# Performance work log

Measured on AMD Instinct MI355X. Metric: run time of the kernel, lower is better.

## Reference

```python
import jax, jax.numpy as jnp
import numpy as np

B, S, V, E, H = 64, 512, 32000, 512, 1024


def setup_inputs() -> dict:
    key = jax.random.key(0)
    ks = jax.random.split(key, 8)
    s = 1.0 / np.sqrt(H).astype(np.float32)
    x = jax.random.randint(ks[0], (B, S), 0, V)  # token ids
    h0 = jnp.zeros((B, H), jnp.float32)
    c0 = jnp.zeros((B, H), jnp.float32)
    emb = jax.random.normal(ks[1], (V, E), jnp.float32) * 0.02
    W_ih = jax.random.uniform(ks[2], (4 * H, E), jnp.float32, -s, s)
    W_hh = jax.random.uniform(ks[3], (4 * H, H), jnp.float32, -s, s)
    b_ih = jax.random.uniform(ks[4], (4 * H,), jnp.float32, -s, s)
    b_hh = jax.random.uniform(ks[5], (4 * H,), jnp.float32, -s, s)
    fc_w = jax.random.uniform(ks[6], (1, H), jnp.float32, -s, s)
    fc_b = jax.random.uniform(ks[7], (1,), jnp.float32, -s, s)
    return {"x": x, "h0": h0, "c0": c0, "emb": emb, "W_ih": W_ih,
            "W_hh": W_hh, "b_ih": b_ih, "b_hh": b_hh, "fc_w": fc_w, "fc_b": fc_b}


def reference(x, h0, c0, emb, W_ih, W_hh, b_ih, b_hh, fc_w, fc_b):
    embeds = emb[x]                      # [B, S, E]
    xs = jnp.swapaxes(embeds, 0, 1)      # [S, B, E] for scan over time
    # precompute input projections for all timesteps in one big GEMM
    xproj = jnp.einsum('sbe,ge->sbg', xs, W_ih) + b_ih  # [S, B, 4H]

    def step(carry, xg):
        h, c = carry
        gates = xg + h @ W_hh.T + b_hh   # [B, 4H], torch LSTMCell gate order i,f,g,o
        i, f, g, o = jnp.split(gates, 4, axis=-1)
        c2 = jax.nn.sigmoid(f) * c + jax.nn.sigmoid(i) * jnp.tanh(g)
        h2 = jax.nn.sigmoid(o) * jnp.tanh(c2)
        return (h2, c2), None

    (h, c), _ = jax.lax.scan(step, (h0, c0), xproj)
    # dropout is identity in eval mode
    out = h @ fc_w.T + fc_b              # [B, 1]
    sig = jax.nn.sigmoid(out)
    sig_out = sig.reshape(x.shape[0], -1)[:, -1]  # [B]
    return (sig_out, h, c)
```

## Files before the change

### kernel.cpp

```cpp
#include <hip/hip_runtime.h>

typedef unsigned short u16;
typedef unsigned int   u32;

typedef __bf16 bf16x8 __attribute__((ext_vector_type(8)));
typedef float  f32x4  __attribute__((ext_vector_type(4)));

#define NB   64
#define NS   512
#define NE   512
#define NH   1024
#define NK   1536
#define NV   32000

#define WPKF_BYTES  12582912u
#define HFRAG_BYTES 262144u
#define AEMBF_BYTES 33554432u
#define BSUM_BYTES  16384u
#define BAR_BYTES   32768u

__device__ __forceinline__ u16 f2bf(float f) {
    u32 u = __builtin_bit_cast(u32, f);
    u += 0x7fffu + ((u >> 16) & 1u);
    return (u16)(u >> 16);
}
__device__ __forceinline__ bf16x8 pack8(float4 a, float4 b) {
    union { u16 u[8]; bf16x8 v; } o;
    o.u[0]=f2bf(a.x); o.u[1]=f2bf(a.y); o.u[2]=f2bf(a.z); o.u[3]=f2bf(a.w);
    o.u[4]=f2bf(b.x); o.u[5]=f2bf(b.y); o.u[6]=f2bf(b.z); o.u[7]=f2bf(b.w);
    return o.v;
}
__device__ __forceinline__ float sigf(float x) {
    return __frcp_rn(1.0f + __expf(-x));
}
__device__ __forceinline__ float tanhf_fast(float x) {
    return 1.0f - 2.0f * __frcp_rn(__expf(2.0f * x) + 1.0f);
}
__device__ __forceinline__ int clamptok(int t) {
    return t < 0 ? 0 : (t >= NV ? NV - 1 : t);
}

__global__ void __launch_bounds__(256)
prep_fused(const int* __restrict__ x, const float* __restrict__ emb,
           const float* __restrict__ Wih, const float* __restrict__ Whh,
           const float* __restrict__ bih, const float* __restrict__ bhh,
           const float* __restrict__ h0,
           u16* __restrict__ wpkf, u16* __restrict__ aembf,
           u16* __restrict__ hfrag0, float* __restrict__ bsum,
           unsigned* __restrict__ bar, int tierA)
{
    const int b = blockIdx.x, t = threadIdx.x;
    if (b < 3072) {
        int oblk = b * 2 + (t >> 7);
        int ot   = t & 127;
        int cg = oblk / 48, kt = oblk % 48;
        int f = ot >> 6, lane = ot & 63;
        int n16 = lane & 15, quad = lane >> 4;
        int nl = f * 16 + n16;
        int j = (nl >> 3) * NH + cg * 8 + (nl & 7);
        int k = kt * 32 + quad * 8;
        const float* src = (k < NH) ? (Whh + (size_t)j * NH + k)
                                    : (Wih + (size_t)j * NE + (k - NH));
        union { bf16x8 v; uint4 q; } o;
        o.v = pack8(*(const float4*)src, *(const float4*)(src + 4));
        *(uint4*)(wpkf + (((size_t)oblk * 2 + f) * 64 + lane) * 8) = o.q;
    } else if (b < 5120) {
        if (!tierA) return;
        int oblk = b - 3072;
        int s = oblk >> 2, bg = oblk & 3;
#pragma unroll
        for (int i = 0; i < 4; ++i) {
            int u = t + i * 256;
            int kt16 = u >> 6, lane = u & 63;
            int n16 = lane & 15, quad = lane >> 4;
            int bb = bg * 16 + n16;
            int tok = clamptok(x[bb * NS + s]);
            const float* ep = emb + (size_t)tok * NE + kt16 * 32 + quad * 8;
            union { bf16x8 v; uint4 q; } o;
            o.v = pack8(*(const float4*)ep, *(const float4*)(ep + 4));
            *(uint4*)(aembf + (((size_t)oblk * 16 + kt16) * 64 + lane) * 8) = o.q;
        }
    } else if (b < 5152) {
        int oblk = (b - 5120) * 4 + (t >> 6);
        int lane = t & 63;
        int bg = oblk >> 5, kt = oblk & 31;
        int n16 = lane & 15, quad = lane >> 4;
        int bb = bg * 16 + n16;
        int k = kt * 32 + quad * 8;
        const float* src = h0 + (size_t)bb * NH + k;
        union { bf16x8 v; uint4 q; } o;
        o.v = pack8(*(const float4*)src, *(const float4*)(src + 4));
        *(uint4*)(hfrag0 + ((size_t)oblk * 64 + lane) * 8) = o.q;
    } else {
        int i = (b - 5152) * 256 + t;
        bsum[i] = bih[i] + bhh[i];
        bar[i] = 0u;
        bar[i + 4096] = 0u;
    }
}

__global__ void init_state(const float* __restrict__ h0,
                           const float* __restrict__ c0,
                           float* __restrict__ out) {
    int i = blockIdx.x * 256 + threadIdx.x;
    float* out_h = out + 64;
    float* out_c = out + 64 + NB * NH;
    ((float4*)out_h)[i] = ((const float4*)h0)[i];
    ((float4*)out_c)[i] = ((const float4*)c0)[i];
}

template<bool EMBF>
__device__ __forceinline__ void persist_body(
    const int* __restrict__ x, const float* __restrict__ emb,
    const u16* __restrict__ wpkf, const u16* __restrict__ aembf,
    u16* __restrict__ hf0, u16* __restrict__ hf1,
    const float* __restrict__ bsum, const float* __restrict__ c0,
    float* __restrict__ cstate, float* __restrict__ out_h,
    unsigned* __restrict__ bar)
{
    const int tid  = threadIdx.x;
    const int lane = tid & 63;
    const int w    = tid >> 6;
    const int blk  = blockIdx.x;
    const int cg   = blk & 127;
    const int bgp  = blk >> 7;
    const int quad = lane >> 4;
    const int n16  = lane & 15;

    __shared__ u16   lw[48 * 2 * 64 * 8];
    __shared__ float part[4][32][36];

    {
        const uint4* src = (const uint4*)(wpkf + (size_t)cg * (48 * 2 * 64 * 8));
        uint4* dst = (uint4*)lw;
#pragma unroll
        for (int i = 0; i < 24; ++i)
            dst[i * 256 + tid] = src[i * 256 + tid];
    }

    const int mloc = tid >> 3;
    const int uu   = tid & 7;
    const int be   = bgp * 32 + mloc;
    const int je   = cg * 8 + uu;
    const float bp0 = bsum[0 * NH + je];
    const float bp1 = bsum[1 * NH + je];
    const float bp2 = bsum[2 * NH + je];
    const float bp3 = bsum[3 * NH + je];
    float c_reg = c0[(size_t)be * NH + je];

    const int kth   = cg >> 2;
    const int lane2 = (cg & 3) * 16 + (mloc & 15);
    const int bgW   = bgp * 2 + (mloc >> 4);
    const size_t hwo_base = ((size_t)(bgW * 32 + kth) * 64 + lane2) * 8;

    const int bg0 = bgp * 2, bg1 = bg0 + 1;

    unsigned* my_flag = bar + ((size_t)(bgp * 128 + cg) * 32);
    const unsigned* pw_flag =
        bar + ((size_t)(bgp * 128 + w * 32 + (lane & 31)) * 32);

    bf16x8 ea0[4], ea1[4];
    auto loadE = [&](int s) {
        if (EMBF) {
            const u16* e0 = aembf + ((size_t)(s * 4 + bg0) * 16) * (64 * 8);
            const u16* e1 = aembf + ((size_t)(s * 4 + bg1) * 16) * (64 * 8);
#pragma unroll
            for (int i = 0; i < 4; ++i) {
                int ke = w * 4 + i;
                ea0[i] = *(const bf16x8*)(e0 + ((size_t)ke * 64 + lane) * 8);
                ea1[i] = *(const bf16x8*)(e1 + ((size_t)ke * 64 + lane) * 8);
            }
        } else {
            int t0 = clamptok(x[(bg0 * 16 + n16) * NS + s]);
            int t1 = clamptok(x[(bg1 * 16 + n16) * NS + s]);
            const float* p0 = emb + (size_t)t0 * NE + quad * 8;
            const float* p1 = emb + (size_t)t1 * NE + quad * 8;
#pragma unroll
            for (int i = 0; i < 4; ++i) {
                int ko = (w * 4 + i) * 32;
                ea0[i] = pack8(*(const float4*)(p0 + ko), *(const float4*)(p0 + ko + 4));
                ea1[i] = pack8(*(const float4*)(p1 + ko), *(const float4*)(p1 + ko + 4));
            }
        }
    };
    loadE(0);
    __syncthreads();

#pragma unroll 1
    for (int s = 0; s < NS; ++s) {
        const u16* hb = (s & 1) ? hf1 : hf0;
        u16*       ho = (s & 1) ? hf0 : hf1;
        const u16* hb0 = hb + (size_t)(bg0 * 32) * (64 * 8);
        const u16* hb1 = hb + (size_t)(bg1 * 32) * (64 * 8);

        f32x4 acc00 = {0.f,0.f,0.f,0.f}, acc01 = {0.f,0.f,0.f,0.f};
        f32x4 acc10 = {0.f,0.f,0.f,0.f}, acc11 = {0.f,0.f,0.f,0.f};

        uint4 hv0[8], hv1[8];
#pragma unroll
        for (int i = 0; i < 8; ++i) {
            const u16* a0p = hb0 + ((size_t)((w * 8 + i) * 64 + lane)) * 8;
            const u16* a1p = hb1 + ((size_t)((w * 8 + i) * 64 + lane)) * 8;
            asm volatile("global_load_dwordx4 %0, %1, off sc0 sc1"
                         : "=v"(hv0[i]) : "v"(a0p) : "memory");
            asm volatile("global_load_dwordx4 %0, %1, off sc0 sc1"
                         : "=v"(hv1[i]) : "v"(a1p) : "memory");
        }

#pragma unroll
        for (int i = 0; i < 4; ++i) {
            int kt = 32 + w * 4 + i;
            bf16x8 w0 = *(const bf16x8*)(lw + ((size_t)(kt * 2 + 0) * 64 + lane) * 8);
            bf16x8 w1 = *(const bf16x8*)(lw + ((size_t)(kt * 2 + 1) * 64 + lane) * 8);
            acc00 = __builtin_amdgcn_mfma_f32_16x16x32_bf16(ea0[i], w0, acc00, 0, 0, 0);
            acc01 = __builtin_amdgcn_mfma_f32_16x16x32_bf16(ea0[i], w1, acc01, 0, 0, 0);
            acc10 = __builtin_amdgcn_mfma_f32_16x16x32_bf16(ea1[i], w0, acc10, 0, 0, 0);
            acc11 = __builtin_amdgcn_mfma_f32_16x16x32_bf16(ea1[i], w1, acc11, 0, 0, 0);
        }

        asm volatile("s_waitcnt vmcnt(0)" ::: "memory");
        __builtin_amdgcn_sched_barrier(0);

#pragma unroll
        for (int i = 0; i < 8; ++i) {
            int kt = w * 8 + i;
            bf16x8 a0 = __builtin_bit_cast(bf16x8, hv0[i]);
            bf16x8 a1 = __builtin_bit_cast(bf16x8, hv1[i]);
            bf16x8 w0 = *(const bf16x8*)(lw + ((size_t)(kt * 2 + 0) * 64 + lane) * 8);
            bf16x8 w1 = *(const bf16x8*)(lw + ((size_t)(kt * 2 + 1) * 64 + lane) * 8);
            acc00 = __builtin_amdgcn_mfma_f32_16x16x32_bf16(a0, w0, acc00, 0, 0, 0);
            acc01 = __builtin_amdgcn_mfma_f32_16x16x32_bf16(a0, w1, acc01, 0, 0, 0);
            acc10 = __builtin_amdgcn_mfma_f32_16x16x32_bf16(a1, w0, acc10, 0, 0, 0);
            acc11 = __builtin_amdgcn_mfma_f32_16x16x32_bf16(a1, w1, acc11, 0, 0, 0);
        }

        {
            int mrow = quad * 4;
#pragma unroll
            for (int r = 0; r < 4; ++r) {
                part[w][mrow + r][n16]           = acc00[r];
                part[w][mrow + r][16 + n16]      = acc01[r];
                part[w][16 + mrow + r][n16]      = acc10[r];
                part[w][16 + mrow + r][16 + n16] = acc11[r];
            }
        }
        __syncthreads();

        float hN;
        {
            float gv0 = bp0, gv1 = bp1, gv2 = bp2, gv3 = bp3;
#pragma unroll
            for (int ww = 0; ww < 4; ++ww) {
                gv0 += part[ww][mloc][ 0 + uu];
                gv1 += part[ww][mloc][ 8 + uu];
                gv2 += part[ww][mloc][16 + uu];
                gv3 += part[ww][mloc][24 + uu];
            }
            float iS = sigf(gv0);
            float fS = sigf(gv1);
            float gT = tanhf_fast(gv2);
            float oS = sigf(gv3);
            float c_new = fS * c_reg + iS * gT;
            c_new = fminf(20.0f, fmaxf(-20.0f, c_new));
            c_reg = c_new;
            hN = oS * tanhf_fast(c_new);
        }

        if (s == NS - 1) {
            out_h[(size_t)be * NH + je]  = hN;
            cstate[(size_t)be * NH + je] = c_reg;
        } else {
            const unsigned need = (unsigned)(s + 1);
            u32 hbf = f2bf(hN);
            u32 hup = (u32)__shfl_down((int)hbf, 1);
            if ((uu & 1) == 0) {
                u32 val = hbf | (hup << 16);
                u32* dst = (u32*)(ho + hwo_base + uu);
                __hip_atomic_store(dst, val, __ATOMIC_RELAXED,
                                   __HIP_MEMORY_SCOPE_AGENT);
            }
            asm volatile("s_waitcnt vmcnt(0)" ::: "memory");
            __syncthreads();
            if (tid == 0)
                __hip_atomic_store(my_flag, need, __ATOMIC_RELAXED,
                                   __HIP_MEMORY_SCOPE_AGENT);
            {
                unsigned v;
                while (true) {
                    asm volatile("global_load_dword %0, %1, off sc0 sc1\n\t"
                                 "s_waitcnt vmcnt(0)"
                                 : "=v"(v) : "v"(pw_flag) : "memory");
                    if (__all(v >= need)) break;
                    __builtin_amdgcn_s_sleep(1);
                }
            }
            loadE(s + 1);
        }
    }
}

__global__ void __launch_bounds__(256, 1)
lstm_persist_a(const int* __restrict__ x, const float* __restrict__ emb,
               const u16* __restrict__ wpkf, const u16* __restrict__ aembf,
               u16* __restrict__ hf0, u16* __restrict__ hf1,
               const float* __restrict__ bsum, const float* __restrict__ c0,
               float* __restrict__ cstate, float* __restrict__ out_h,
               unsigned* __restrict__ bar) {
    persist_body<true>(x, emb, wpkf, aembf, hf0, hf1, bsum, c0, cstate, out_h, bar);
}

__global__ void __launch_bounds__(256, 1)
lstm_persist_b(const int* __restrict__ x, const float* __restrict__ emb,
               const u16* __restrict__ wpkf, const u16* __restrict__ aembf,
               u16* __restrict__ hf0, u16* __restrict__ hf1,
               const float* __restrict__ bsum, const float* __restrict__ c0,
               float* __restrict__ cstate, float* __restrict__ out_h,
               unsigned* __restrict__ bar) {
    persist_body<false>(x, emb, wpkf, aembf, hf0, hf1, bsum, c0, cstate, out_h, bar);
}

__global__ void __launch_bounds__(256)
lstm_step_raw(const int* __restrict__ x, const float* __restrict__ emb,
              const float* __restrict__ Wih, const float* __restrict__ Whh,
              const float* __restrict__ bih, const float* __restrict__ bhh,
              const float* __restrict__ hA, float* __restrict__ hB,
              float* __restrict__ cbuf, int s) {
    const int tid  = threadIdx.x;
    const int lane = tid & 63;
    const int w    = tid >> 6;
    const int blk  = blockIdx.x;
    const int cg   = blk & 127;
    const int bg   = blk >> 7;
    const int u0   = cg * 8;
    const int b0   = bg * 16;

    __shared__ float part[4][16][36];
    const int n16 = lane & 15;
    const int kq  = (lane >> 4) * 8;
    const int tok = clamptok(x[(b0 + n16) * NS + s]);

    const int nl0 = n16, nl1 = 16 + n16;
    const int r0 = (nl0 >> 3) * NH + u0 + (nl0 & 7);
    const int r1 = (nl1 >> 3) * NH + u0 + (nl1 & 7);

    f32x4 acc0 = {0.f,0.f,0.f,0.f};
    f32x4 acc1 = {0.f,0.f,0.f,0.f};

#pragma unroll
    for (int tkt = 0; tkt < 12; ++tkt) {
        int kt = w * 12 + tkt;
        int ko = kt * 32 + kq;
        const float *s0, *s1;
        if (kt < 32) { s0 = Whh + (size_t)r0 * NH + ko; s1 = Whh + (size_t)r1 * NH + ko; }
        else         { s0 = Wih + (size_t)r0 * NE + (ko - NH); s1 = Wih + (size_t)r1 * NE + (ko - NH); }
        bf16x8 wf0 = pack8(*(const float4*)s0, *(const float4*)(s0 + 4));
        bf16x8 wf1 = pack8(*(const float4*)s1, *(const float4*)(s1 + 4));
        bf16x8 a0;
        if (kt < 32) {
            const float* hp = hA + (size_t)(b0 + n16) * NH + ko;
            a0 = pack8(*(const float4*)hp, *(const float4*)(hp + 4));
        } else {
            const float* ep = emb + (size_t)tok * NE + (ko - NH);
            a0 = pack8(*(const float4*)ep, *(const float4*)(ep + 4));
        }
        acc0 = __builtin_amdgcn_mfma_f32_16x16x32_bf16(a0, wf0, acc0, 0, 0, 0);
        acc1 = __builtin_amdgcn_mfma_f32_16x16x32_bf16(a0, wf1, acc1, 0, 0, 0);
    }

    {
        int mrow = (lane >> 4) * 4;
#pragma unroll
        for (int r = 0; r < 4; ++r) {
            part[w][mrow + r][n16]      = acc0[r];
            part[w][mrow + r][16 + n16] = acc1[r];
        }
    }
    __syncthreads();

    if (tid < 128) {
        const int mloc = tid >> 3, uu = tid & 7;
        const int be = b0 + mloc, je = u0 + uu;
        float gv[4];
#pragma unroll
        for (int g = 0; g < 4; ++g) {
            int n = g * 8 + uu;
            gv[g] = part[0][mloc][n] + part[1][mloc][n]
                  + part[2][mloc][n] + part[3][mloc][n]
                  + bih[g * NH + je] + bhh[g * NH + je];
        }
        float iS = sigf(gv[0]);
        float fS = sigf(gv[1]);
        float gT = tanhf_fast(gv[2]);
        float oS = sigf(gv[3]);
        float c_new = fS * cbuf[be * NH + je] + iS * gT;
        c_new = fminf(20.0f, fmaxf(-20.0f, c_new));
        float hN = oS * tanhf_fast(c_new);
        cbuf[be * NH + je] = c_new;
        hB[be * NH + je]   = hN;
    }
}

__global__ void final_fc_simple(const float* __restrict__ fc_w,
                                const float* __restrict__ fc_b,
                                float* __restrict__ out) {
    __shared__ float red[64][5];
    const float* out_h = out + 64;
    int t = threadIdx.x;
    int b = t >> 2, q = t & 3;
    const float* hp = out_h + b * NH + q * 256;
    const float* wp = fc_w + q * 256;
    float sacc = 0.f;
#pragma unroll 4
    for (int i = 0; i < 64; ++i) {
        float4 hv = ((const float4*)hp)[i];
        float4 wv = ((const float4*)wp)[i];
        sacc += hv.x * wv.x + hv.y * wv.y + hv.z * wv.z + hv.w * wv.w;
    }
    red[b][q] = sacc;
    __syncthreads();
    if (q == 0) {
        float tot = red[b][0] + red[b][1] + red[b][2] + red[b][3] + fc_b[0];
        out[b] = 1.0f / (1.0f + expf(-tot));
    }
}

extern "C" void kernel_launch(void* const* d_in, const int* in_sizes, int n_in,
                              void* d_out, int out_size, void* d_ws, size_t ws_size,
                              hipStream_t stream) {
    const int*   x   = (const int*)d_in[0];
    const float* h0  = (const float*)d_in[1];
    const float* c0  = (const float*)d_in[2];
    const float* emb = (const float*)d_in[3];
    const float* Wih = (const float*)d_in[4];
    const float* Whh = (const float*)d_in[5];
    const float* bih = (const float*)d_in[6];
    const float* bhh = (const float*)d_in[7];
    const float* fcw = (const float*)d_in[8];
    const float* fcb = (const float*)d_in[9];

    float* out   = (float*)d_out;
    float* out_h = out + 64;
    float* out_c = out + 64 + NB * NH;

    const size_t needA = (size_t)WPKF_BYTES + HFRAG_BYTES + AEMBF_BYTES + BSUM_BYTES + BAR_BYTES;
    const size_t needB = (size_t)WPKF_BYTES + HFRAG_BYTES + BSUM_BYTES + BAR_BYTES;
    const bool tierA = ws_size >= needA;
    const bool tierB = !tierA && ws_size >= needB;

    if (tierA || tierB) {
        u16* wpkf  = (u16*)d_ws;
        u16* hfrag = (u16*)((char*)d_ws + WPKF_BYTES);
        u16* hf0 = hfrag;
        u16* hf1 = hfrag + HFRAG_BYTES / 4;
        char* after = (char*)d_ws + WPKF_BYTES + HFRAG_BYTES;
        u16*   aembf = tierA ? (u16*)after : nullptr;
        float* bsum  = (float*)(after + (tierA ? AEMBF_BYTES : 0));
        unsigned* bar = (unsigned*)((char*)bsum + BSUM_BYTES);

        hipLaunchKernelGGL(prep_fused, dim3(5168), dim3(256), 0, stream,
                           x, emb, Wih, Whh, bih, bhh, h0,
                           wpkf, aembf, hf0, bsum, bar, (int)tierA);

        void* kargs[11] = { &x, &emb, &wpkf, &aembf, &hf0, &hf1,
                            &bsum, &c0, &out_c, &out_h, &bar };
        (void)hipLaunchCooperativeKernel(
            tierA ? reinterpret_cast<const void*>(&lstm_persist_a)
                  : reinterpret_cast<const void*>(&lstm_persist_b),
            dim3(256), dim3(256), kargs, 0u, stream);
    } else {
        hipLaunchKernelGGL(init_state, dim3(64), dim3(256), 0, stream, h0, c0, out);
        float* wsH = (float*)d_ws;
        for (int s = 0; s < NS; ++s) {
            const float* hA = (s & 1) ? wsH : out_h;
            float*       hB = (s & 1) ? out_h : wsH;
            hipLaunchKernelGGL(lstm_step_raw, dim3(512), dim3(256), 0, stream,
                               x, emb, Wih, Whh, bih, bhh, hA, hB, out_c, s);
        }
    }

    hipLaunchKernelGGL(final_fc_simple, dim3(1), dim3(256), 0, stream,
                       fcw, fcb, out);
}
```

Before: 2.046 ms.

## Replace block barrier before flag publish with per-wave flags and double-buffered partials

Each wave now publishes its own readiness flag right after its h stores, instead of a block-wide __syncthreads followed by a single-thread flag store. Consumers read four per-wave flags with one dwordx4 load. The LDS partial-sum buffer is double-buffered by step parity so that dropping the barrier does not create a write-after-read hazard. The next step's embedding load is also issued before the spin-wait so its latency overlaps with it. The intent is to cut one block barrier per timestep on the serial recurrence critical path, at the cost of more flag traffic and more LDS.

```diff
diff --git a/kernel.cpp b/kernel.cpp
--- a/kernel.cpp
+++ b/kernel.cpp
@@ -128,7 +128,7 @@
     const int n16  = lane & 15;
 
     __shared__ u16   lw[48 * 2 * 64 * 8];
-    __shared__ float part[4][32][36];
+    __shared__ float part[2][4][32][36];
 
     {
         const uint4* src = (const uint4*)(wpkf + (size_t)cg * (48 * 2 * 64 * 8));
@@ -155,7 +155,7 @@
 
     const int bg0 = bgp * 2, bg1 = bg0 + 1;
 
-    unsigned* my_flag = bar + ((size_t)(bgp * 128 + cg) * 32);
+    unsigned* myw_flag = bar + ((size_t)(bgp * 128 + cg) * 32) + w;
     const unsigned* pw_flag =
         bar + ((size_t)(bgp * 128 + w * 32 + (lane & 31)) * 32);
 
@@ -192,6 +192,7 @@
         u16*       ho = (s & 1) ? hf0 : hf1;
         const u16* hb0 = hb + (size_t)(bg0 * 32) * (64 * 8);
         const u16* hb1 = hb + (size_t)(bg1 * 32) * (64 * 8);
+        float (*pcur)[32][36] = part[s & 1];
 
         f32x4 acc00 = {0.f,0.f,0.f,0.f}, acc01 = {0.f,0.f,0.f,0.f};
         f32x4 acc10 = {0.f,0.f,0.f,0.f}, acc11 = {0.f,0.f,0.f,0.f};
@@ -238,10 +239,10 @@
             int mrow = quad * 4;
 #pragma unroll
             for (int r = 0; r < 4; ++r) {
-                part[w][mrow + r][n16]           = acc00[r];
-                part[w][mrow + r][16 + n16]      = acc01[r];
-                part[w][16 + mrow + r][n16]      = acc10[r];
-                part[w][16 + mrow + r][16 + n16] = acc11[r];
+                pcur[w][mrow + r][n16]           = acc00[r];
+                pcur[w][mrow + r][16 + n16]      = acc01[r];
+                pcur[w][16 + mrow + r][n16]      = acc10[r];
+                pcur[w][16 + mrow + r][16 + n16] = acc11[r];
             }
         }
         __syncthreads();
@@ -251,10 +252,10 @@
             float gv0 = bp0, gv1 = bp1, gv2 = bp2, gv3 = bp3;
 #pragma unroll
             for (int ww = 0; ww < 4; ++ww) {
-                gv0 += part[ww][mloc][ 0 + uu];
-                gv1 += part[ww][mloc][ 8 + uu];
-                gv2 += part[ww][mloc][16 + uu];
-                gv3 += part[ww][mloc][24 + uu];
+                gv0 += pcur[ww][mloc][ 0 + uu];
+                gv1 += pcur[ww][mloc][ 8 + uu];
+                gv2 += pcur[ww][mloc][16 + uu];
+                gv3 += pcur[ww][mloc][24 + uu];
             }
             float iS = sigf(gv0);
             float fS = sigf(gv1);
@@ -280,21 +281,21 @@
                                    __HIP_MEMORY_SCOPE_AGENT);
             }
             asm volatile("s_waitcnt vmcnt(0)" ::: "memory");
-            __syncthreads();
-            if (tid == 0)
-                __hip_atomic_store(my_flag, need, __ATOMIC_RELAXED,
+            if (lane == 0)
+                __hip_atomic_store(myw_flag, need, __ATOMIC_RELAXED,
                                    __HIP_MEMORY_SCOPE_AGENT);
+            loadE(s + 1);
             {
-                unsigned v;
+                uint4 v;
                 while (true) {
-                    asm volatile("global_load_dword %0, %1, off sc0 sc1\n\t"
+                    asm volatile("global_load_dwordx4 %0, %1, off sc0 sc1\n\t"
                                  "s_waitcnt vmcnt(0)"
                                  : "=v"(v) : "v"(pw_flag) : "memory");
-                    if (__all(v >= need)) break;
+                    if (__all(v.x >= need && v.y >= need &&
+                              v.z >= need && v.w >= need)) break;
                     __builtin_amdgcn_s_sleep(1);
                 }
             }
-            loadE(s + 1);
         }
     }
 }
```

Result: no change. 2.033 ms (-0.7%).
